# Kernel tuning notes

Measured on AMD Instinct MI355X. Metric: run time of the kernel, lower is better.

Reference implementation:

```python
import jax, jax.numpy as jnp
import numpy as np

N = 200_000          # active voxels
C = 64               # in/out channels
K = 3                # kernel size per dim
SHAPE = (128, 128, 128)  # spatial grid (D, H, W)
B = 2                # batch size
KV = K ** 3          # 27 kernel offsets


def setup_inputs() -> dict:
    key = jax.random.key(0)
    kb, kz, ky, kx, kf, k0, k1 = jax.random.split(key, 7)
    b = jax.random.randint(kb, (N, 1), 0, B, dtype=jnp.int32)
    z = jax.random.randint(kz, (N, 1), 0, SHAPE[0], dtype=jnp.int32)
    y = jax.random.randint(ky, (N, 1), 0, SHAPE[1], dtype=jnp.int32)
    x = jax.random.randint(kx, (N, 1), 0, SHAPE[2], dtype=jnp.int32)
    coors = jnp.concatenate([b, z, y, x], axis=1)  # [N, 4] (batch, z, y, x)
    features = jax.random.normal(kf, (N, C), dtype=jnp.float32)
    W0 = jax.random.normal(k0, (KV, C, C), dtype=jnp.float32) * 0.05  # layer 0 weights per offset
    W1 = jax.random.normal(k1, (KV, C, C), dtype=jnp.float32) * 0.05  # layer 1 weights per offset
    return {"features": features, "coors": coors, "W0": W0, "W1": W1, "batch_size": B}


def _neighbor_indices(coors, batch_size):
    """Rulebook: for each of the 27 kernel offsets, index of the active input
    voxel feeding each active output voxel, or -1 if that neighbor is inactive."""
    D, H, W = SHAPE
    n = coors.shape[0]
    # dense coord -> row-index hash grid
    flat = ((coors[:, 0] * D + coors[:, 1]) * H + coors[:, 2]) * W + coors[:, 3]
    grid = jnp.full((batch_size * D * H * W,), -1, dtype=jnp.int32)
    grid = grid.at[flat].set(jnp.arange(n, dtype=jnp.int32))
    r = K // 2
    ax = jnp.arange(-r, r + 1, dtype=jnp.int32)
    offs = jnp.stack(jnp.meshgrid(ax, ax, ax, indexing="ij"), axis=-1).reshape(-1, 3)  # [27, 3]
    shp = jnp.array(SHAPE, dtype=jnp.int32)
    nb_coord = coors[None, :, 1:] + offs[:, None, :]               # [27, N, 3]
    valid = jnp.all((nb_coord >= 0) & (nb_coord < shp), axis=-1)   # [27, N]
    nc = jnp.clip(nb_coord, 0, shp - 1)
    nflat = ((coors[None, :, 0] * D + nc[..., 0]) * H + nc[..., 1]) * W + nc[..., 2]
    nb = grid[nflat]                                               # [27, N]
    return jnp.where(valid, nb, -1)


def _subm_conv(feats, W, nb):
    # gather -> per-offset GEMM -> accumulate (all offsets fused in one einsum)
    mask = (nb >= 0)
    g = feats[jnp.maximum(nb, 0)] * mask[..., None].astype(feats.dtype)  # [27, N, C]
    return jnp.einsum("knc,kco->no", g, W)  # [N, C]


def reference(features, coors, W0, W1, batch_size):
    coors = coors.astype(jnp.int32)
    nb = _neighbor_indices(coors, batch_size)  # active set is preserved across subm layers
    x = _subm_conv(features, W0, nb)
    return _subm_conv(x, W1, nb)
```

## Files before the change

### kernel.cpp

```cpp
#include <hip/hip_runtime.h>
#include <stdint.h>

#define SD 128
#define SH 128
#define SW 128
#define BATCH 2
#define CCH 64
#define KV 27

typedef __attribute__((ext_vector_type(4))) float f32x4;
typedef __attribute__((ext_vector_type(8))) short s16x8;

__device__ __forceinline__ unsigned short f2bf_rne(float f) {
    union { float f; unsigned int u; } v; v.f = f;
    unsigned int u = v.u;
    return (unsigned short)((u + 0x7FFFu + ((u >> 16) & 1u)) >> 16);
}

__device__ __forceinline__ s16x8 pack_bf8(float4 a, float4 b) {
    s16x8 o;
    o[0] = (short)f2bf_rne(a.x); o[1] = (short)f2bf_rne(a.y);
    o[2] = (short)f2bf_rne(a.z); o[3] = (short)f2bf_rne(a.w);
    o[4] = (short)f2bf_rne(b.x); o[5] = (short)f2bf_rne(b.y);
    o[6] = (short)f2bf_rne(b.z); o[7] = (short)f2bf_rne(b.w);
    return o;
}

__global__ void k_f2bf(const float4* __restrict__ in, ushort4* __restrict__ out, int n4) {
    int i = blockIdx.x * blockDim.x + threadIdx.x;
    if (i >= n4) return;
    float4 a = in[i];
    ushort4 o;
    o.x = f2bf_rne(a.x); o.y = f2bf_rne(a.y);
    o.z = f2bf_rne(a.z); o.w = f2bf_rne(a.w);
    out[i] = o;
}

__global__ void k_wprep(const float* __restrict__ W, unsigned short* __restrict__ Wt) {
    int idx = blockIdx.x * blockDim.x + threadIdx.x;
    if (idx >= KV * CCH * CCH) return;
    int k = idx / (CCH * CCH);
    int rem = idx - k * CCH * CCH;
    int ci = rem >> 6, co = rem & 63;
    int d = ((k * 8 + (ci >> 3)) * 64 + co) * 8 + (ci & 7);
    Wt[d] = f2bf_rne(W[idx]);
}

__global__ void k_scatter(const int4* __restrict__ coors, int* __restrict__ grid, int n) {
    int i = blockIdx.x * blockDim.x + threadIdx.x;
    if (i >= n) return;
    int4 c = coors[i];
    int flat = ((c.x * SD + c.y) * SH + c.z) * SW + c.w;
    atomicMax(&grid[flat], i);
}

template <int IN_F32, int OUT_BF16>
__global__ __launch_bounds__(256) void k_conv(const void* __restrict__ finv,
                                              const s16x8* __restrict__ wt,
                                              const int4* __restrict__ coors,
                                              const int* __restrict__ grid,
                                              void* __restrict__ outp, int n) {
    int wid = blockIdx.x * (blockDim.x >> 6) + (threadIdx.x >> 6);
    int lane = threadIdx.x & 63;
    int base = wid * 32;
    if (base >= n) return;
    int r = lane & 15;
    int g = lane >> 4;

    int li = lane & 31;
    int myrow = base + li;
    int rowok = (myrow < n) ? 1 : 0;
    int4 c = coors[rowok ? myrow : 0];
    int z = c.y, y = c.z, x = c.w;
    int flatbase = ((c.x * SD + z) * SH + y) * SW + x;

    f32x4 acc[2][4] = {};

    auto lookup = [&](int k) -> int {
        int dz = k / 9 - 1, dy = (k / 3) % 3 - 1, dx = k % 3 - 1;
        int zz = z + dz, yy = y + dy, xx = x + dx;
        int v = -1;
        if (rowok && (unsigned)zz < SD && (unsigned)yy < SH && (unsigned)xx < SW)
            v = grid[flatbase + dz * (SH * SW) + dy * SW + dx];
        return v;
    };

    int nbr = lookup(0);
    for (int k = 0; k < KV; ++k) {
        int nbr_next = (k + 1 < KV) ? lookup(k + 1) : -1;
        int nb0 = __shfl(nbr, r);
        int nb1 = __shfl(nbr, 16 + r);
        nbr = nbr_next;
        unsigned long long m0 = __ballot(nb0 >= 0);
        unsigned long long m1 = __ballot(nb1 >= 0);
        if ((m0 | m1) == 0ULL) continue;

        s16x8 bf[2][4];
#pragma unroll
        for (int s = 0; s < 2; ++s)
#pragma unroll
            for (int t = 0; t < 4; ++t)
                bf[s][t] = wt[(k * 8 + s * 4 + g) * 64 + t * 16 + r];

        int nbh[2] = {nb0, nb1};
        unsigned long long mm[2] = {m0, m1};
#pragma unroll
        for (int h = 0; h < 2; ++h) {
            if (!mm[h]) continue;
            int nbx = nbh[h];
            s16x8 a0 = {}, a1 = {};
            if (nbx >= 0) {
                if (IN_F32) {
                    const float4* ff = (const float4*)finv;
                    size_t rb = (size_t)nbx * 16 + g * 2;
                    float4 p0 = ff[rb], p1 = ff[rb + 1];
                    float4 p2 = ff[rb + 8], p3 = ff[rb + 9];
                    a0 = pack_bf8(p0, p1);
                    a1 = pack_bf8(p2, p3);
                } else {
                    const s16x8* fb = (const s16x8*)finv;
                    a0 = fb[(size_t)nbx * 8 + g];
                    a1 = fb[(size_t)nbx * 8 + 4 + g];
                }
            }
#pragma unroll
            for (int t = 0; t < 4; ++t) {
                acc[h][t] = __builtin_amdgcn_mfma_f32_16x16x32_bf16(a0, bf[0][t], acc[h][t], 0, 0, 0);
                acc[h][t] = __builtin_amdgcn_mfma_f32_16x16x32_bf16(a1, bf[1][t], acc[h][t], 0, 0, 0);
            }
        }
    }

    if (OUT_BF16) {
        unsigned short* __restrict__ o = (unsigned short*)outp;
#pragma unroll
        for (int h = 0; h < 2; ++h)
#pragma unroll
            for (int t = 0; t < 4; ++t)
#pragma unroll
                for (int j = 0; j < 4; ++j) {
                    int row = base + h * 16 + g * 4 + j;
                    if (row < n) o[(size_t)row * 64 + t * 16 + r] = f2bf_rne(acc[h][t][j]);
                }
    } else {
        float* __restrict__ o = (float*)outp;
#pragma unroll
        for (int h = 0; h < 2; ++h)
#pragma unroll
            for (int t = 0; t < 4; ++t)
#pragma unroll
                for (int j = 0; j < 4; ++j) {
                    int row = base + h * 16 + g * 4 + j;
                    if (row < n) o[(size_t)row * 64 + t * 16 + r] = acc[h][t][j];
                }
    }
}

extern "C" void kernel_launch(void* const* d_in, const int* in_sizes, int n_in,
                              void* d_out, int out_size, void* d_ws, size_t ws_size,
                              hipStream_t stream) {
    const float* feats = (const float*)d_in[0];
    const int4* coors = (const int4*)d_in[1];
    const float* W0 = (const float*)d_in[2];
    const float* W1 = (const float*)d_in[3];
    int N = in_sizes[0] / CCH;

    char* p = (char*)d_ws;
    auto carve = [&](size_t bytes) -> char* {
        char* q = p;
        p += (bytes + 255) & ~(size_t)255;
        return q;
    };
    size_t grid_bytes = (size_t)BATCH * SD * SH * SW * 4;
    int* grid = (int*)carve(grid_bytes);
    unsigned short* wt0 = (unsigned short*)carve((size_t)KV * CCH * CCH * 2);
    unsigned short* wt1 = (unsigned short*)carve((size_t)KV * CCH * CCH * 2);
    s16x8* ibf = (s16x8*)carve((size_t)N * CCH * 2);
    size_t base_need = (size_t)(p - (char*)d_ws);
    s16x8* fbf = nullptr;
    if (ws_size >= base_need + (size_t)N * CCH * 2 + 256)
        fbf = (s16x8*)carve((size_t)N * CCH * 2);

    hipMemsetAsync(grid, 0xFF, grid_bytes, stream);

    int nw = KV * CCH * CCH;
    k_wprep<<<(nw + 255) / 256, 256, 0, stream>>>(W0, wt0);
    k_wprep<<<(nw + 255) / 256, 256, 0, stream>>>(W1, wt1);
    k_scatter<<<(N + 255) / 256, 256, 0, stream>>>(coors, grid, N);

    int tiles = (N + 31) / 32;
    int blocks = (tiles + 3) / 4;
    if (fbf) {
        int n4 = N * CCH / 4;
        k_f2bf<<<(n4 + 255) / 256, 256, 0, stream>>>((const float4*)feats, (ushort4*)fbf, n4);
        k_conv<0, 1><<<blocks, 256, 0, stream>>>(fbf, (const s16x8*)wt0, coors, grid, ibf, N);
    } else {
        k_conv<1, 1><<<blocks, 256, 0, stream>>>(feats, (const s16x8*)wt0, coors, grid, ibf, N);
    }
    k_conv<0, 0><<<blocks, 256, 0, stream>>>(ibf, (const s16x8*)wt1, coors, grid, d_out, N);
}
```

Before: 305.1 us.

## Sort active voxels into grid order to improve gather locality in sparse conv

Adds a compaction pass (count, scan, compact) that renumbers active voxels in spatial grid order, rewrites the hash grid to hold the sorted indices, and permutes the features into that order as bf16. Both conv layers then run on the sorted rows, so neighbor gathers within a wavefront touch nearby memory, and blocks are remapped across XCDs for cache locality. The final layer scatters its output back through the permutation. This adds several extra kernels and passes over the 16M-cell grid, and duplicate-coordinate handling now relies on a losers pass using an atomic counter.

```diff
diff --git a/kernel.cpp b/kernel.cpp
--- a/kernel.cpp
+++ b/kernel.cpp
@@ -7,6 +7,9 @@
 #define BATCH 2
 #define CCH 64
 #define KV 27
+#define NCELL (BATCH * SD * SH * SW)
+#define CHUNK 4096
+#define NCHUNK (NCELL / CHUNK)
 
 typedef __attribute__((ext_vector_type(4))) float f32x4;
 typedef __attribute__((ext_vector_type(8))) short s16x8;
@@ -25,6 +28,223 @@
     o[6] = (short)f2bf_rne(b.z); o[7] = (short)f2bf_rne(b.w);
     return o;
 }
+
+
+__global__ void k_wprep(const float* __restrict__ W, unsigned short* __restrict__ Wt) {
+    int idx = blockIdx.x * blockDim.x + threadIdx.x;
+    if (idx >= KV * CCH * CCH) return;
+    int k = idx / (CCH * CCH);
+    int rem = idx - k * CCH * CCH;
+    int ci = rem >> 6, co = rem & 63;
+    int d = ((k * 8 + (ci >> 3)) * 64 + co) * 8 + (ci & 7);
+    Wt[d] = f2bf_rne(W[idx]);
+}
+
+__global__ void k_scatter(const int4* __restrict__ coors, int* __restrict__ grid, int n) {
+    int i = blockIdx.x * blockDim.x + threadIdx.x;
+    if (i >= n) return;
+    int4 c = coors[i];
+    int flat = ((c.x * SD + c.y) * SH + c.z) * SW + c.w;
+    atomicMax(&grid[flat], i);
+}
+
+
+__global__ void k_count(const int4* __restrict__ grid4, int* __restrict__ counts) {
+    int t = threadIdx.x;
+    size_t base = (size_t)blockIdx.x * (CHUNK / 4) + t * 4;
+    int cnt = 0;
+#pragma unroll
+    for (int i = 0; i < 4; ++i) {
+        int4 v = grid4[base + i];
+        cnt += (v.x >= 0) + (v.y >= 0) + (v.z >= 0) + (v.w >= 0);
+    }
+    __shared__ int s[256];
+    s[t] = cnt; __syncthreads();
+    for (int d = 128; d > 0; d >>= 1) {
+        if (t < d) s[t] += s[t + d];
+        __syncthreads();
+    }
+    if (t == 0) counts[blockIdx.x] = s[0];
+}
+
+__global__ void k_scan(const int* __restrict__ counts, int* __restrict__ excl, int* __restrict__ ctr) {
+    __shared__ int s[NCHUNK];
+    int t = threadIdx.x;
+    int v = counts[t];
+    s[t] = v; __syncthreads();
+    for (int d = 1; d < NCHUNK; d <<= 1) {
+        int a = (t >= d) ? s[t - d] : 0;
+        __syncthreads();
+        s[t] += a;
+        __syncthreads();
+    }
+    excl[t] = s[t] - v;
+    if (t == NCHUNK - 1) ctr[0] = s[t];
+}
+
+__global__ void k_compact(int* __restrict__ grid, const int* __restrict__ excl,
+                          int* __restrict__ perm) {
+    int t = threadIdx.x;
+    size_t cellbase = (size_t)blockIdx.x * CHUNK + t * 16;
+    int v[16];
+    const int4* g4 = (const int4*)(grid + cellbase);
+#pragma unroll
+    for (int i = 0; i < 4; ++i) {
+        int4 a = g4[i];
+        v[i * 4 + 0] = a.x; v[i * 4 + 1] = a.y; v[i * 4 + 2] = a.z; v[i * 4 + 3] = a.w;
+    }
+    int cnt = 0;
+#pragma unroll
+    for (int i = 0; i < 16; ++i) cnt += (v[i] >= 0);
+    __shared__ int s[256];
+    s[t] = cnt; __syncthreads();
+    for (int d = 1; d < 256; d <<= 1) {
+        int a = (t >= d) ? s[t - d] : 0;
+        __syncthreads();
+        s[t] += a;
+        __syncthreads();
+    }
+    int idx = excl[blockIdx.x] + s[t] - cnt;
+#pragma unroll
+    for (int i = 0; i < 16; ++i) {
+        if (v[i] >= 0) {
+            perm[idx] = v[i];
+            grid[cellbase + i] = idx;
+            idx++;
+        }
+    }
+}
+
+__global__ void k_losers(const int4* __restrict__ coors, const int* __restrict__ grid,
+                         int* __restrict__ perm, int* __restrict__ ctr, int n) {
+    int j = blockIdx.x * blockDim.x + threadIdx.x;
+    if (j >= n) return;
+    int4 c = coors[j];
+    int flat = ((c.x * SD + c.y) * SH + c.z) * SW + c.w;
+    int si = grid[flat];
+    if (perm[si] != j) {
+        int s = atomicAdd(ctr, 1);
+        perm[s] = j;
+    }
+}
+
+__global__ void k_permfeat(const float4* __restrict__ feats4, const int4* __restrict__ coors,
+                           const int* __restrict__ perm, s16x8* __restrict__ fs,
+                           int* __restrict__ fb, int n) {
+    int tid = blockIdx.x * blockDim.x + threadIdx.x;
+    int i = tid >> 3, j = tid & 7;
+    if (i >= n) return;
+    int src = perm[i];
+    float4 p0 = feats4[(size_t)src * 16 + j * 2];
+    float4 p1 = feats4[(size_t)src * 16 + j * 2 + 1];
+    fs[(size_t)i * 8 + j] = pack_bf8(p0, p1);
+    if (j == 0) {
+        int4 c = coors[src];
+        fb[i] = ((c.x * SD + c.y) * SH + c.z) * SW + c.w;
+    }
+}
+
+template <int OUT_PERM>
+__global__ __launch_bounds__(256) void k_conv_s(const s16x8* __restrict__ fin,
+                                                const s16x8* __restrict__ wt,
+                                                const int* __restrict__ fb,
+                                                const int* __restrict__ grid,
+                                                const int* __restrict__ perm,
+                                                void* __restrict__ outp, int n) {
+    int nwg = gridDim.x, orig = blockIdx.x;
+    int q = nwg >> 3, rr = nwg & 7;
+    int xcd = orig & 7, bidx = orig >> 3;
+    int blk = (xcd < rr ? xcd * (q + 1) : rr * (q + 1) + (xcd - rr) * q) + bidx;
+
+    int wid = blk * (blockDim.x >> 6) + (threadIdx.x >> 6);
+    int lane = threadIdx.x & 63;
+    int base = wid * 32;
+    if (base >= n) return;
+    int r = lane & 15;
+    int g = lane >> 4;
+    int li = lane & 31;
+    int myrow = base + li;
+    int rowok = (myrow < n) ? 1 : 0;
+    int fbv = fb[rowok ? myrow : 0];
+    int pl = 0;
+    if (OUT_PERM) pl = rowok ? perm[myrow] : 0;
+    int z = (fbv >> 14) & 127, y = (fbv >> 7) & 127, x = fbv & 127;
+
+    f32x4 acc[2][4] = {};
+
+    auto lookup = [&](int k) -> int {
+        int dz = k / 9 - 1, dy = (k / 3) % 3 - 1, dx = k % 3 - 1;
+        int zz = z + dz, yy = y + dy, xx = x + dx;
+        int v = -1;
+        if (rowok && (unsigned)zz < SD && (unsigned)yy < SH && (unsigned)xx < SW)
+            v = grid[fbv + dz * (SH * SW) + dy * SW + dx];
+        return v;
+    };
+
+    int nbr = lookup(0);
+    for (int k = 0; k < KV; ++k) {
+        int nbr_next = (k + 1 < KV) ? lookup(k + 1) : -1;
+        int nb0 = __shfl(nbr, r);
+        int nb1 = __shfl(nbr, 16 + r);
+        nbr = nbr_next;
+        unsigned long long m0 = __ballot(nb0 >= 0);
+        unsigned long long m1 = __ballot(nb1 >= 0);
+        if ((m0 | m1) == 0ULL) continue;
+
+        s16x8 bf[2][4];
+#pragma unroll
+        for (int s = 0; s < 2; ++s)
+#pragma unroll
+            for (int t = 0; t < 4; ++t)
+                bf[s][t] = wt[(k * 8 + s * 4 + g) * 64 + t * 16 + r];
+
+        int nbh[2] = {nb0, nb1};
+        unsigned long long mm[2] = {m0, m1};
+#pragma unroll
+        for (int h = 0; h < 2; ++h) {
+            if (!mm[h]) continue;
+            int nbx = nbh[h];
+            s16x8 a0 = {}, a1 = {};
+            if (nbx >= 0) {
+                a0 = fin[(size_t)nbx * 8 + g];
+                a1 = fin[(size_t)nbx * 8 + 4 + g];
+            }
+#pragma unroll
+            for (int t = 0; t < 4; ++t) {
+                acc[h][t] = __builtin_amdgcn_mfma_f32_16x16x32_bf16(a0, bf[0][t], acc[h][t], 0, 0, 0);
+                acc[h][t] = __builtin_amdgcn_mfma_f32_16x16x32_bf16(a1, bf[1][t], acc[h][t], 0, 0, 0);
+            }
+        }
+    }
+
+    if (OUT_PERM) {
+        float* __restrict__ o = (float*)outp;
+#pragma unroll
+        for (int h = 0; h < 2; ++h)
+#pragma unroll
+            for (int t = 0; t < 4; ++t)
+#pragma unroll
+                for (int j = 0; j < 4; ++j) {
+                    int w = h * 16 + g * 4 + j;
+                    if (base + w < n) {
+                        int orow = __shfl(pl, w);
+                        o[(size_t)orow * 64 + t * 16 + r] = acc[h][t][j];
+                    }
+                }
+    } else {
+        unsigned short* __restrict__ o = (unsigned short*)outp;
+#pragma unroll
+        for (int h = 0; h < 2; ++h)
+#pragma unroll
+            for (int t = 0; t < 4; ++t)
+#pragma unroll
+                for (int j = 0; j < 4; ++j) {
+                    int row = base + h * 16 + g * 4 + j;
+                    if (row < n) o[(size_t)row * 64 + t * 16 + r] = f2bf_rne(acc[h][t][j]);
+                }
+    }
+}
+
 
 __global__ void k_f2bf(const float4* __restrict__ in, ushort4* __restrict__ out, int n4) {
     int i = blockIdx.x * blockDim.x + threadIdx.x;
@@ -36,37 +256,18 @@
     out[i] = o;
 }
 
-__global__ void k_wprep(const float* __restrict__ W, unsigned short* __restrict__ Wt) {
-    int idx = blockIdx.x * blockDim.x + threadIdx.x;
-    if (idx >= KV * CCH * CCH) return;
-    int k = idx / (CCH * CCH);
-    int rem = idx - k * CCH * CCH;
-    int ci = rem >> 6, co = rem & 63;
-    int d = ((k * 8 + (ci >> 3)) * 64 + co) * 8 + (ci & 7);
-    Wt[d] = f2bf_rne(W[idx]);
-}
-
-__global__ void k_scatter(const int4* __restrict__ coors, int* __restrict__ grid, int n) {
-    int i = blockIdx.x * blockDim.x + threadIdx.x;
-    if (i >= n) return;
-    int4 c = coors[i];
-    int flat = ((c.x * SD + c.y) * SH + c.z) * SW + c.w;
-    atomicMax(&grid[flat], i);
-}
-
 template <int IN_F32, int OUT_BF16>
-__global__ __launch_bounds__(256) void k_conv(const void* __restrict__ finv,
-                                              const s16x8* __restrict__ wt,
-                                              const int4* __restrict__ coors,
-                                              const int* __restrict__ grid,
-                                              void* __restrict__ outp, int n) {
+__global__ __launch_bounds__(256) void k_conv_legacy(const void* __restrict__ finv,
+                                                     const s16x8* __restrict__ wt,
+                                                     const int4* __restrict__ coors,
+                                                     const int* __restrict__ grid,
+                                                     void* __restrict__ outp, int n) {
     int wid = blockIdx.x * (blockDim.x >> 6) + (threadIdx.x >> 6);
     int lane = threadIdx.x & 63;
     int base = wid * 32;
     if (base >= n) return;
     int r = lane & 15;
     int g = lane >> 4;
-
     int li = lane & 31;
     int myrow = base + li;
     int rowok = (myrow < n) ? 1 : 0;
@@ -118,9 +319,9 @@
                     a0 = pack_bf8(p0, p1);
                     a1 = pack_bf8(p2, p3);
                 } else {
-                    const s16x8* fb = (const s16x8*)finv;
-                    a0 = fb[(size_t)nbx * 8 + g];
-                    a1 = fb[(size_t)nbx * 8 + 4 + g];
+                    const s16x8* fbp = (const s16x8*)finv;
+                    a0 = fbp[(size_t)nbx * 8 + g];
+                    a1 = fbp[(size_t)nbx * 8 + 4 + g];
                 }
             }
 #pragma unroll
@@ -165,37 +366,60 @@
     const float* W1 = (const float*)d_in[3];
     int N = in_sizes[0] / CCH;
 
-    char* p = (char*)d_ws;
+    char* p0 = (char*)d_ws;
+    char* p = p0;
     auto carve = [&](size_t bytes) -> char* {
         char* q = p;
         p += (bytes + 255) & ~(size_t)255;
         return q;
     };
-    size_t grid_bytes = (size_t)BATCH * SD * SH * SW * 4;
+
+    size_t grid_bytes = (size_t)NCELL * 4;
     int* grid = (int*)carve(grid_bytes);
     unsigned short* wt0 = (unsigned short*)carve((size_t)KV * CCH * CCH * 2);
     unsigned short* wt1 = (unsigned short*)carve((size_t)KV * CCH * CCH * 2);
-    s16x8* ibf = (s16x8*)carve((size_t)N * CCH * 2);
-    size_t base_need = (size_t)(p - (char*)d_ws);
-    s16x8* fbf = nullptr;
-    if (ws_size >= base_need + (size_t)N * CCH * 2 + 256)
-        fbf = (s16x8*)carve((size_t)N * CCH * 2);
+
+    char* psave = p;
+    int* counts = (int*)carve(NCHUNK * 4);
+    int* excl = (int*)carve(NCHUNK * 4);
+    int* ctr = (int*)carve(256);
+    int* perm = (int*)carve((size_t)N * 4);
+    int* fb = (int*)carve((size_t)N * 4);
+    s16x8* fs = (s16x8*)carve((size_t)N * CCH * 2);
+    s16x8* ibf_s = (s16x8*)carve((size_t)N * CCH * 2);
+    bool sorted_ok = (size_t)(p - p0) <= ws_size;
+
+    int nw = KV * CCH * CCH;
+    int tiles = (N + 31) / 32;
+    int blocks = (tiles + 3) / 4;
 
     hipMemsetAsync(grid, 0xFF, grid_bytes, stream);
-
-    int nw = KV * CCH * CCH;
     k_wprep<<<(nw + 255) / 256, 256, 0, stream>>>(W0, wt0);
     k_wprep<<<(nw + 255) / 256, 256, 0, stream>>>(W1, wt1);
     k_scatter<<<(N + 255) / 256, 256, 0, stream>>>(coors, grid, N);
 
-    int tiles = (N + 31) / 32;
-    int blocks = (tiles + 3) / 4;
-    if (fbf) {
-        int n4 = N * CCH / 4;
-        k_f2bf<<<(n4 + 255) / 256, 256, 0, stream>>>((const float4*)feats, (ushort4*)fbf, n4);
-        k_conv<0, 1><<<blocks, 256, 0, stream>>>(fbf, (const s16x8*)wt0, coors, grid, ibf, N);
+    if (sorted_ok) {
+        k_count<<<NCHUNK, 256, 0, stream>>>((const int4*)grid, counts);
+        k_scan<<<1, NCHUNK, 0, stream>>>(counts, excl, ctr);
+        k_compact<<<NCHUNK, 256, 0, stream>>>(grid, excl, perm);
+        k_losers<<<(N + 255) / 256, 256, 0, stream>>>(coors, grid, perm, ctr, N);
+        k_permfeat<<<((N * 8) + 255) / 256, 256, 0, stream>>>((const float4*)feats, coors, perm, fs, fb, N);
+        k_conv_s<0><<<blocks, 256, 0, stream>>>(fs, (const s16x8*)wt0, fb, grid, perm, ibf_s, N);
+        k_conv_s<1><<<blocks, 256, 0, stream>>>(ibf_s, (const s16x8*)wt1, fb, grid, perm, d_out, N);
     } else {
-        k_conv<1, 1><<<blocks, 256, 0, stream>>>(feats, (const s16x8*)wt0, coors, grid, ibf, N);
-    }
-    k_conv<0, 0><<<blocks, 256, 0, stream>>>(ibf, (const s16x8*)wt1, coors, grid, d_out, N);
-}
+        p = psave;
+        s16x8* ibf = (s16x8*)carve((size_t)N * CCH * 2);
+        size_t base_need = (size_t)(p - p0);
+        s16x8* fbf = nullptr;
+        if (ws_size >= base_need + (size_t)N * CCH * 2 + 256)
+            fbf = (s16x8*)carve((size_t)N * CCH * 2);
+        if (fbf) {
+            int n4 = N * CCH / 4;
+            k_f2bf<<<(n4 + 255) / 256, 256, 0, stream>>>((const float4*)feats, (ushort4*)fbf, n4);
+            k_conv_legacy<0, 1><<<blocks, 256, 0, stream>>>(fbf, (const s16x8*)wt0, coors, grid, ibf, N);
+        } else {
+            k_conv_legacy<1, 1><<<blocks, 256, 0, stream>>>(feats, (const s16x8*)wt0, coors, grid, ibf, N);
+        }
+        k_conv_legacy<0, 0><<<blocks, 256, 0, stream>>>(ibf, (const s16x8*)wt1, coors, grid, d_out, N);
+    }
+}
```

Result: slower. 318.7 us (+4.5%).
